# Kernel optimization log

Hardware: AMD Instinct MI355X
Metric: run time of the kernel (lower is better)

Reference implementation:

```python
import jax, jax.numpy as jnp
import numpy as np

TOP_K = 8
NEG_SLOPE = 0.2  # PyG GATConv default negative_slope


def setup_inputs() -> dict:
    key = jax.random.key(0)
    ks = jax.random.split(key, 8)
    B, C, T, D, H, KD = 16, 64, 128, 256, 8, 32
    s = 1.0 / np.sqrt(D)
    return {
        "x": jax.random.normal(ks[0], (B, C, T, D), jnp.float32),
        "static_adj": jax.random.normal(ks[1], (C, C), jnp.float32),
        "w_q": jax.random.normal(ks[2], (KD, D), jnp.float32) * s,
        "w_k": jax.random.normal(ks[3], (KD, D), jnp.float32) * s,
        "gat_lin": jax.random.normal(ks[4], (H * D, D), jnp.float32) * s,  # shared lin_src/lin_dst
        "att_src": jax.random.normal(ks[5], (H, D), jnp.float32) * s,
        "att_dst": jax.random.normal(ks[6], (H, D), jnp.float32) * s,
        "gat_bias": jnp.zeros((D,), jnp.float32),
    }


def reference(x, static_adj, w_q, w_k, gat_lin, att_src, att_dst, gat_bias):
    B, C, T, D = x.shape
    H = att_src.shape[0]
    kd = w_q.shape[0]

    # ---- dynamic adjacency ----
    h = x.mean(axis=2)                                   # [B,C,D] temporal summary
    q = h @ w_q.T                                        # [B,C,KD]
    k = h @ w_k.T                                        # [B,C,KD]
    sim = jnp.einsum('bik,bjk->bij', q, k) / np.float32(np.sqrt(kd))
    delta_a = jnp.tanh(sim)                              # [B,C,C]
    adaptive = static_adj[None] + delta_a                # [B,C,C]

    # top-k per row -> sparse mask (edge: row i = source, col j = target, per dense_to_sparse)
    _, idx = jax.lax.top_k(jnp.abs(adaptive), TOP_K)     # [B,C,K]
    mask = jnp.any(jax.nn.one_hot(idx, C, dtype=bool), axis=-2)  # [B,C,C]
    mask = mask | jnp.eye(C, dtype=bool)                 # GATConv add_self_loops=True

    # ---- GAT message passing (dense masked attention, graph shared across T) ----
    xt = jnp.swapaxes(x, 1, 2)                           # [B,T,C,D]
    wx = (xt @ gat_lin.T).reshape(B, T, C, H, D)         # [B,T,C,H,F]
    a_s = jnp.einsum('btchf,hf->btch', wx, att_src)      # source term
    a_d = jnp.einsum('btchf,hf->btch', wx, att_dst)      # target term
    # e[b,t,i,j,h]: edge source i -> target j
    e = a_s[:, :, :, None, :] + a_d[:, :, None, :, :]
    e = jax.nn.leaky_relu(e, NEG_SLOPE)
    e = jnp.where(mask[:, None, :, :, None], e, -jnp.inf)
    alpha = jax.nn.softmax(e, axis=2)                    # softmax over incoming sources i per target j
    out = jnp.einsum('btijh,btihf->btjhf', alpha, wx)    # aggregate messages
    out = out.mean(axis=3) + gat_bias                    # concat=False -> mean heads, add bias
    x_updated = jnp.swapaxes(out, 1, 2)                  # [B,C,T,D]
    return x_updated, delta_a
```

## Files before the change

### kernel.cpp

```cpp
#include <hip/hip_runtime.h>

typedef _Float16 h2_t __attribute__((ext_vector_type(2)));
typedef _Float16 h4_t __attribute__((ext_vector_type(4)));
typedef _Float16 h8_t __attribute__((ext_vector_type(8)));
typedef __fp16 fp16x2 __attribute__((ext_vector_type(2)));
typedef float f32x16 __attribute__((ext_vector_type(16)));


__device__ __forceinline__ h2_t pkrtz(float a, float b) {
  union { fp16x2 f; h2_t h; } u;
  u.f = __builtin_amdgcn_cvt_pkrtz(a, b);
  return u.h;
}

__device__ __forceinline__ unsigned pk_u(float a, float b) {
  union { fp16x2 f; unsigned u; } z;
  z.f = __builtin_amdgcn_cvt_pkrtz(a, b);
  return z.u;
}

__device__ __forceinline__ h8_t mk8(unsigned w0, unsigned w1, unsigned w2, unsigned w3) {
  union { unsigned u[4]; h8_t h; } z;
  z.u[0] = w0; z.u[1] = w1; z.u[2] = w2; z.u[3] = w3;
  return z.h;
}

__device__ __forceinline__ float fdot2_(h2_t a, h2_t b, float c) {
#if __has_builtin(__builtin_amdgcn_fdot2)
  return __builtin_amdgcn_fdot2(a, b, c, false);
#else
  return fmaf((float)a[0], (float)b[0], fmaf((float)a[1], (float)b[1], c));
#endif
}

__device__ __forceinline__ h2_t u2h(unsigned u) {
  union { unsigned u; h2_t h; } x; x.u = u; return x.h;
}

__global__ void k_hmean(const float* __restrict__ x, float* __restrict__ h) {
  int bc = blockIdx.x;
  int d = threadIdx.x;
  const float* xp = x + (size_t)bc * (128 * 256) + d;
  float s = 0.f;
  #pragma unroll 8
  for (int t = 0; t < 128; ++t) s += xp[(size_t)t * 256];
  h[bc * 256 + d] = s * (1.f / 128.f);
}

__global__ void k_qk(const float* __restrict__ h, const float* __restrict__ wq,
                     const float* __restrict__ wk, float* __restrict__ q,
                     float* __restrict__ k) {
  int gid = blockIdx.x * 256 + threadIdx.x;
  int isK = gid >> 15;
  int e = gid & 32767;
  int kk = e & 31;
  int bi = e >> 5;
  const float4* h4 = (const float4*)(h + bi * 256);
  const float4* w4 = (const float4*)((isK ? wk : wq) + kk * 256);
  float s = 0.f;
  #pragma unroll 4
  for (int d = 0; d < 64; ++d) {
    float4 a = h4[d], bv = w4[d];
    s = fmaf(a.x, bv.x, s); s = fmaf(a.y, bv.y, s);
    s = fmaf(a.z, bv.z, s); s = fmaf(a.w, bv.w, s);
  }
  (isK ? k : q)[e] = s;
}

__global__ void k_adj(const float* __restrict__ q, const float* __restrict__ k,
                      const float* __restrict__ sadj, float* __restrict__ dout,
                      unsigned long long* __restrict__ cmask) {
  __shared__ float qs[64][33], ks[64][33];
  __shared__ float ad[64][65];
  __shared__ unsigned long long rowm[64];
  int b = blockIdx.x, tid = threadIdx.x;
  for (int r = 0; r < 8; ++r) {
    int idx = r * 256 + tid;
    qs[idx >> 5][idx & 31] = q[b * 2048 + idx];
    ks[idx >> 5][idx & 31] = k[b * 2048 + idx];
  }
  __syncthreads();
  const float rs = 0.17677669529663687f;
  for (int r = 0; r < 16; ++r) {
    int idx = r * 256 + tid;
    int i = idx >> 6, j = idx & 63;
    float s = 0.f;
    #pragma unroll 8
    for (int kk = 0; kk < 32; ++kk) s = fmaf(qs[i][kk], ks[j][kk], s);
    float dv = tanhf(s * rs);
    dout[b * 4096 + idx] = dv;
    ad[i][j] = sadj[idx] + dv;
  }
  __syncthreads();
  if (tid < 64) {
    unsigned long long sel = 0ull;
    for (int p = 0; p < 8; ++p) {
      float best = -1.f; int bj = 0;
      for (int j = 0; j < 64; ++j) {
        if ((sel >> j) & 1ull) continue;
        float v = fabsf(ad[tid][j]);
        if (v > best) { best = v; bj = j; }
      }
      sel |= 1ull << bj;
    }
    rowm[tid] = sel;
  }
  __syncthreads();
  if (tid < 64) {
    unsigned long long cmv = 1ull << tid;
    for (int i = 0; i < 64; ++i) cmv |= ((rowm[i] >> tid) & 1ull) << i;
    cmask[b * 64 + tid] = cmv;
  }
}

__global__ void k_vsd(const float* __restrict__ glin, const float* __restrict__ asrc,
                      const float* __restrict__ adst, _Float16* __restrict__ vsd16) {
  int hh = blockIdx.x, d = threadIdx.x;
  const float* gb = glin + (size_t)hh * 65536;
  float s = 0.f, t = 0.f;
  for (int f = 0; f < 256; ++f) {
    float g = gb[f * 256 + d];
    s = fmaf(asrc[hh * 256 + f], g, s);
    t = fmaf(adst[hh * 256 + f], g, t);
  }
  vsd16[hh * 256 + d] = (_Float16)s;
  vsd16[(8 + hh) * 256 + d] = (_Float16)t;
}

__global__ void k_grearr(const float* __restrict__ g, _Float16* __restrict__ o) {
  int gid = blockIdx.x * 256 + threadIdx.x;
  int lane = gid & 63;
  int fg = (gid >> 6) & 3;
  int FID = gid >> 8;
  int ft = FID & 1, kk = (FID >> 1) & 3, s = FID >> 3;
  int h = s >> 2, dc = s & 3;
  int l5 = lane & 31, hi = lane >> 5;
  int f = fg * 64 + ft * 32 + l5;
  int d0 = dc * 64 + kk * 16 + hi * 8;
  const float* src = g + ((size_t)(h * 256 + f) << 8) + d0;
  float4 a = *(const float4*)src;
  float4 bq = *(const float4*)(src + 4);
  h8_t v;
  v[0] = (_Float16)a.x;  v[1] = (_Float16)a.y;  v[2] = (_Float16)a.z;  v[3] = (_Float16)a.w;
  v[4] = (_Float16)bq.x; v[5] = (_Float16)bq.y; v[6] = (_Float16)bq.z; v[7] = (_Float16)bq.w;
  *(h8_t*)(o + (size_t)gid * 8) = v;
}

__global__ __launch_bounds__(512) void k_main(
    const float* __restrict__ x, const _Float16* __restrict__ vsd16,
    const unsigned long long* __restrict__ cmask,
    const _Float16* __restrict__ g16r, const float* __restrict__ bias,
    float* __restrict__ out)
{
  __shared__ __align__(16) char LDS[69632];
  char* XR  = LDS;
  char* PT  = LDS;
  char* RED = LDS;
  float* ASp = (float*)(LDS + 65536);
  float* ADp = (float*)(LDS + 67584);

  const int tid = threadIdx.x;
  const int lane = tid & 63;
  const int w = __builtin_amdgcn_readfirstlane(tid >> 6);
  const int hi = lane >> 5;
  const int l5 = lane & 31;
  const int l7 = lane & 7;
  const int mg = w & 1;
  const int fg = w >> 1;
  const int bt = blockIdx.x;
  const int b = bt >> 7, t = bt & 127;

  const char* gb0 = (const char*)g16r + fg * 1024 + lane * 16;

  h8_t GA[8], GB[8];
  #pragma unroll
  for (int q = 0; q < 8; ++q) GA[q] = *(const h8_t*)(gb0 + q * 4096);

  #pragma unroll
  for (int r = 0; r < 8; ++r) {
    int i = w * 8 + r;
    const float4 v = *(const float4*)(x + (((size_t)(b * 64 + i) * 128 + t) << 8) + lane * 4);
    h2_t p0 = pkrtz(v.x, v.y);
    h2_t p1 = pkrtz(v.z, v.w);
    h4_t hv; hv[0] = p0[0]; hv[1] = p0[1]; hv[2] = p1[0]; hv[3] = p1[1];
    int db = lane >> 1;
    int off = i * 512 + (((db & 24) | ((db ^ (i & 7)) & 7)) << 4) + ((lane & 1) << 3);
    *(h4_t*)(XR + off) = hv;
  }
  __syncthreads();

  h8_t Af[16];
  {
    int i = mg * 32 + l5;
    #pragma unroll
    for (int k = 0; k < 16; ++k) {
      int db = k * 2 + hi;
      Af[k] = *(const h8_t*)(XR + i * 512 + (((db & 24) | ((db ^ l7) & 7)) << 4));
    }
  }

  {
    float a_s = 0.f, a_d = 0.f;
    const unsigned* vsp = (const unsigned*)vsd16 + w * 128;
    const unsigned* vdp = (const unsigned*)vsd16 + (8 + w) * 128;
    #pragma unroll 4
    for (int db = 0; db < 32; ++db) {
      h8_t xv = *(const h8_t*)(XR + lane * 512 + (((db & 24) | ((db ^ l7) & 7)) << 4));
      #pragma unroll
      for (int c = 0; c < 4; ++c) {
        h2_t x2; x2[0] = xv[c * 2]; x2[1] = xv[c * 2 + 1];
        a_s = fdot2_(x2, u2h(vsp[db * 4 + c]), a_s);
        a_d = fdot2_(x2, u2h(vdp[db * 4 + c]), a_d);
      }
    }
    ASp[w * 64 + lane] = a_s;
    ADp[w * 64 + lane] = a_d;
  }
  __syncthreads();

  {
    const unsigned long long cmj = cmask[b * 64 + lane];
    const float adj = ADp[w * 64 + lane];
    const float* asr = ASp + w * 64;
    float ssum = 0.f;
    #pragma unroll 8
    for (int i = 0; i < 64; ++i) {
      float e = asr[i] + adj;
      e = fmaxf(e, 0.f) + 0.2f * fminf(e, 0.f);
      e = ((cmj >> i) & 1ull) ? e : -1e30f;
      ssum += exp2f(e * 1.44269504f);
    }
    const float rinv = 1.f / ssum;
    #pragma unroll
    for (int c = 0; c < 8; ++c) {
      float vv[8];
      #pragma unroll
      for (int e8 = 0; e8 < 8; ++e8) {
        int i = c * 8 + e8;
        float e = asr[i] + adj;
        e = fmaxf(e, 0.f) + 0.2f * fminf(e, 0.f);
        e = ((cmj >> i) & 1ull) ? e : -1e30f;
        vv[e8] = exp2f(e * 1.44269504f) * rinv;
      }
      *(h8_t*)(PT + w * 8192 + lane * 128 + ((c ^ l7) << 4)) =
          mk8(pk_u(vv[0], vv[1]), pk_u(vv[2], vv[3]),
              pk_u(vv[4], vv[5]), pk_u(vv[6], vv[7]));
    }
  }
  __syncthreads();

  f32x16 acc00 = {}, acc01 = {}, acc10 = {}, acc11 = {};

  #pragma unroll 1
  for (int h = 0; h < 8; ++h) {
    f32x16 d0 = {}, d1 = {};

    #pragma unroll
    for (int dc = 0; dc < 4; ++dc) {
      const int s = h * 4 + dc;
      const int sp = (s < 31) ? s + 1 : 31;
      const char* gpp = gb0 + (size_t)sp * 32768;
      if ((dc & 1) == 0) {
        #pragma unroll
        for (int q = 0; q < 8; ++q) GB[q] = *(const h8_t*)(gpp + q * 4096);
        #pragma unroll
        for (int kk = 0; kk < 4; ++kk) {
          d0 = __builtin_amdgcn_mfma_f32_32x32x16_f16(Af[dc * 4 + kk], GA[kk * 2 + 0], d0, 0, 0, 0);
          d1 = __builtin_amdgcn_mfma_f32_32x32x16_f16(Af[dc * 4 + kk], GA[kk * 2 + 1], d1, 0, 0, 0);
        }
      } else {
        #pragma unroll
        for (int q = 0; q < 8; ++q) GA[q] = *(const h8_t*)(gpp + q * 4096);
        #pragma unroll
        for (int kk = 0; kk < 4; ++kk) {
          d0 = __builtin_amdgcn_mfma_f32_32x32x16_f16(Af[dc * 4 + kk], GB[kk * 2 + 0], d0, 0, 0, 0);
          d1 = __builtin_amdgcn_mfma_f32_32x32x16_f16(Af[dc * 4 + kk], GB[kk * 2 + 1], d1, 0, 0, 0);
        }
      }
    }

    h8_t B2[2][2];
    {
      const bool H = (hi != 0);
      #pragma unroll
      for (int ft = 0; ft < 2; ++ft) {
        const f32x16& dd = ft ? d1 : d0;
        unsigned P0 = pk_u(dd[0], dd[1]),  P1 = pk_u(dd[2], dd[3]);
        unsigned P2 = pk_u(dd[4], dd[5]),  P3 = pk_u(dd[6], dd[7]);
        unsigned P4 = pk_u(dd[8], dd[9]),  P5 = pk_u(dd[10], dd[11]);
        unsigned P6 = pk_u(dd[12], dd[13]), P7 = pk_u(dd[14], dd[15]);
        {
          unsigned Pa = H ? P2 : P0, Pb = H ? P3 : P1;
          unsigned Qa = H ? P0 : P2, Qb = H ? P1 : P3;
          unsigned S0 = (unsigned)__shfl_xor((int)Qa, 32);
          unsigned S1 = (unsigned)__shfl_xor((int)Qb, 32);
          B2[0][ft] = mk8(H ? S0 : Pa, H ? S1 : Pb, H ? Pa : S0, H ? Pb : S1);
        }
        {
          unsigned Pa = H ? P6 : P4, Pb = H ? P7 : P5;
          unsigned Qa = H ? P4 : P6, Qb = H ? P5 : P7;
          unsigned S0 = (unsigned)__shfl_xor((int)Qa, 32);
          unsigned S1 = (unsigned)__shfl_xor((int)Qb, 32);
          B2[1][ft] = mk8(H ? S0 : Pa, H ? S1 : Pb, H ? Pa : S0, H ? Pb : S1);
        }
      }
    }

    h8_t A2[2][2];
    #pragma unroll
    for (int jt = 0; jt < 2; ++jt)
      #pragma unroll
      for (int kbl = 0; kbl < 2; ++kbl) {
        int c = mg * 4 + kbl * 2 + hi;
        A2[jt][kbl] = *(const h8_t*)(PT + h * 8192 + (jt * 32 + l5) * 128 + ((c ^ (l5 & 7)) << 4));
      }

    acc00 = __builtin_amdgcn_mfma_f32_32x32x16_f16(A2[0][0], B2[0][0], acc00, 0, 0, 0);
    acc00 = __builtin_amdgcn_mfma_f32_32x32x16_f16(A2[0][1], B2[1][0], acc00, 0, 0, 0);
    acc01 = __builtin_amdgcn_mfma_f32_32x32x16_f16(A2[0][0], B2[0][1], acc01, 0, 0, 0);
    acc01 = __builtin_amdgcn_mfma_f32_32x32x16_f16(A2[0][1], B2[1][1], acc01, 0, 0, 0);
    acc10 = __builtin_amdgcn_mfma_f32_32x32x16_f16(A2[1][0], B2[0][0], acc10, 0, 0, 0);
    acc10 = __builtin_amdgcn_mfma_f32_32x32x16_f16(A2[1][1], B2[1][0], acc10, 0, 0, 0);
    acc11 = __builtin_amdgcn_mfma_f32_32x32x16_f16(A2[1][0], B2[0][1], acc11, 0, 0, 0);
    acc11 = __builtin_amdgcn_mfma_f32_32x32x16_f16(A2[1][1], B2[1][1], acc11, 0, 0, 0);
  }

  __syncthreads();
  if (mg == 1) {
    #pragma unroll
    for (int jt = 0; jt < 2; ++jt)
      #pragma unroll
      for (int ft = 0; ft < 2; ++ft) {
        const f32x16& a = jt ? (ft ? acc11 : acc10) : (ft ? acc01 : acc00);
        #pragma unroll
        for (int rq = 0; rq < 4; ++rq) {
          float4 v; v.x = a[rq*4+0]; v.y = a[rq*4+1]; v.z = a[rq*4+2]; v.w = a[rq*4+3];
          *(float4*)(RED + (((((fg*2+jt)*2+ft)*4 + rq)*64 + lane) << 4)) = v;
        }
      }
  }
  __syncthreads();
  if (mg == 0) {
    const float bi0 = bias[fg * 64 + l5];
    const float bi1 = bias[fg * 64 + 32 + l5];
    float* ob = out + ((size_t)(b * 64) * 128 + t) * 256;
    #pragma unroll
    for (int jt = 0; jt < 2; ++jt)
      #pragma unroll
      for (int ft = 0; ft < 2; ++ft) {
        const f32x16& a = jt ? (ft ? acc11 : acc10) : (ft ? acc01 : acc00);
        const float bv = ft ? bi1 : bi0;
        const int fcol = fg * 64 + ft * 32 + l5;
        #pragma unroll
        for (int rq = 0; rq < 4; ++rq) {
          float4 p = *(const float4*)(RED + (((((fg*2+jt)*2+ft)*4 + rq)*64 + lane) << 4));
          #pragma unroll
          for (int rr = 0; rr < 4; ++rr) {
            int j = jt * 32 + rr + 8 * rq + 4 * hi;
            float sum = a[rq*4+rr] + ((const float*)&p)[rr];
            ob[(size_t)j * 32768 + fcol] = sum * 0.125f + bv;
          }
        }
      }
  }
}

extern "C" void kernel_launch(void* const* d_in, const int* in_sizes, int n_in,
                              void* d_out, int out_size, void* d_ws, size_t ws_size,
                              hipStream_t stream) {
  const float* x    = (const float*)d_in[0];
  const float* sadj = (const float*)d_in[1];
  const float* wq   = (const float*)d_in[2];
  const float* wk   = (const float*)d_in[3];
  const float* glin = (const float*)d_in[4];
  const float* asrc = (const float*)d_in[5];
  const float* adst = (const float*)d_in[6];
  const float* bias = (const float*)d_in[7];

  float* out = (float*)d_out;
  float* delta_out = out + (size_t)16 * 64 * 128 * 256;

  char* ws = (char*)d_ws;
  float* h   = (float*)(ws + 0);
  float* q   = (float*)(ws + 1048576);
  float* k   = (float*)(ws + 1179648);
  unsigned long long* cm = (unsigned long long*)(ws + 1310720);
  _Float16* vsd16 = (_Float16*)(ws + 1318912);
  _Float16* g16r  = (_Float16*)(ws + 1327104);

  hipLaunchKernelGGL(k_hmean,  dim3(1024), dim3(256), 0, stream, x, h);
  hipLaunchKernelGGL(k_qk,     dim3(256),  dim3(256), 0, stream, h, wq, wk, q, k);
  hipLaunchKernelGGL(k_adj,    dim3(16),   dim3(256), 0, stream, q, k, sadj, delta_out, cm);
  hipLaunchKernelGGL(k_vsd,    dim3(8),    dim3(256), 0, stream, glin, asrc, adst, vsd16);
  hipLaunchKernelGGL(k_grearr, dim3(256),  dim3(256), 0, stream, glin, g16r);
  hipLaunchKernelGGL(k_main,   dim3(2048), dim3(512), 0, stream, x, vsd16, cm, g16r, bias, out);
}
```

Measured before the change: 361.3 us.

## Process two timesteps per block, each wave pair owning one timestep

```diff
diff --git a/kernel.cpp b/kernel.cpp
--- a/kernel.cpp
+++ b/kernel.cpp
@@ -152,12 +152,11 @@
     const _Float16* __restrict__ g16r, const float* __restrict__ bias,
     float* __restrict__ out)
 {
-  __shared__ __align__(16) char LDS[69632];
-  char* XR  = LDS;
-  char* PT  = LDS;
-  char* RED = LDS;
-  float* ASp = (float*)(LDS + 65536);
-  float* ADp = (float*)(LDS + 67584);
+  __shared__ __align__(16) char LDS[139264];
+  char* XT  = LDS;
+  char* PT  = LDS + 65536;
+  float* ASp = (float*)(LDS + 131072);
+  float* ADp = (float*)(LDS + 135168);
 
   const int tid = threadIdx.x;
   const int lane = tid & 63;
@@ -165,10 +164,12 @@
   const int hi = lane >> 5;
   const int l5 = lane & 31;
   const int l7 = lane & 7;
-  const int mg = w & 1;
+  const int tg = w & 1;
   const int fg = w >> 1;
   const int bt = blockIdx.x;
-  const int b = bt >> 7, t = bt & 127;
+  const int b = bt >> 6;
+  const int t0 = (bt & 63) * 2;
+  const int t = t0 + tg;
 
   const char* gb0 = (const char*)g16r + fg * 1024 + lane * 16;
 
@@ -176,174 +177,186 @@
   #pragma unroll
   for (int q = 0; q < 8; ++q) GA[q] = *(const h8_t*)(gb0 + q * 4096);
 
-  #pragma unroll
-  for (int r = 0; r < 8; ++r) {
-    int i = w * 8 + r;
-    const float4 v = *(const float4*)(x + (((size_t)(b * 64 + i) * 128 + t) << 8) + lane * 4);
-    h2_t p0 = pkrtz(v.x, v.y);
-    h2_t p1 = pkrtz(v.z, v.w);
-    h4_t hv; hv[0] = p0[0]; hv[1] = p0[1]; hv[2] = p1[0]; hv[3] = p1[1];
-    int db = lane >> 1;
-    int off = i * 512 + (((db & 24) | ((db ^ (i & 7)) & 7)) << 4) + ((lane & 1) << 3);
-    *(h4_t*)(XR + off) = hv;
+  const unsigned long long cmj = cmask[b * 64 + lane];
+
+  {
+    char* XL = XT + tg * 32768;
+    const int rb = fg * 16;
+    #pragma unroll
+    for (int r = 0; r < 16; ++r) {
+      int i = rb + r;
+      const float4 v = *(const float4*)(x + (((size_t)(b * 64 + i) * 128 + t) << 8) + lane * 4);
+      h2_t p0 = pkrtz(v.x, v.y);
+      h2_t p1 = pkrtz(v.z, v.w);
+      h4_t hv; hv[0] = p0[0]; hv[1] = p0[1]; hv[2] = p1[0]; hv[3] = p1[1];
+      int db = lane >> 1;
+      int off = i * 512 + (((db & 24) | ((db ^ (i & 7)) & 7)) << 4) + ((lane & 1) << 3);
+      *(h4_t*)(XL + off) = hv;
+    }
   }
   __syncthreads();
 
-  h8_t Af[16];
   {
-    int i = mg * 32 + l5;
-    #pragma unroll
-    for (int k = 0; k < 16; ++k) {
-      int db = k * 2 + hi;
-      Af[k] = *(const h8_t*)(XR + i * 512 + (((db & 24) | ((db ^ l7) & 7)) << 4));
-    }
-  }
-
-  {
-    float a_s = 0.f, a_d = 0.f;
-    const unsigned* vsp = (const unsigned*)vsd16 + w * 128;
-    const unsigned* vdp = (const unsigned*)vsd16 + (8 + w) * 128;
+    const char* XL = XT + tg * 32768;
+    const int hp = w >> 1;
+    float s0 = 0.f, d0v = 0.f, s1 = 0.f, d1v = 0.f;
+    const unsigned* vsp0 = (const unsigned*)vsd16 + hp * 128;
+    const unsigned* vdp0 = (const unsigned*)vsd16 + (8 + hp) * 128;
+    const unsigned* vsp1 = (const unsigned*)vsd16 + (hp + 4) * 128;
+    const unsigned* vdp1 = (const unsigned*)vsd16 + (12 + hp) * 128;
     #pragma unroll 4
     for (int db = 0; db < 32; ++db) {
-      h8_t xv = *(const h8_t*)(XR + lane * 512 + (((db & 24) | ((db ^ l7) & 7)) << 4));
+      h8_t xv = *(const h8_t*)(XL + lane * 512 + (((db & 24) | ((db ^ l7) & 7)) << 4));
       #pragma unroll
       for (int c = 0; c < 4; ++c) {
         h2_t x2; x2[0] = xv[c * 2]; x2[1] = xv[c * 2 + 1];
-        a_s = fdot2_(x2, u2h(vsp[db * 4 + c]), a_s);
-        a_d = fdot2_(x2, u2h(vdp[db * 4 + c]), a_d);
+        s0  = fdot2_(x2, u2h(vsp0[db * 4 + c]), s0);
+        d0v = fdot2_(x2, u2h(vdp0[db * 4 + c]), d0v);
+        s1  = fdot2_(x2, u2h(vsp1[db * 4 + c]), s1);
+        d1v = fdot2_(x2, u2h(vdp1[db * 4 + c]), d1v);
       }
     }
-    ASp[w * 64 + lane] = a_s;
-    ADp[w * 64 + lane] = a_d;
+    ASp[tg * 512 + hp * 64 + lane] = s0;
+    ADp[tg * 512 + hp * 64 + lane] = d0v;
+    ASp[tg * 512 + (hp + 4) * 64 + lane] = s1;
+    ADp[tg * 512 + (hp + 4) * 64 + lane] = d1v;
   }
   __syncthreads();
 
-  {
-    const unsigned long long cmj = cmask[b * 64 + lane];
-    const float adj = ADp[w * 64 + lane];
-    const float* asr = ASp + w * 64;
-    float ssum = 0.f;
-    #pragma unroll 8
-    for (int i = 0; i < 64; ++i) {
-      float e = asr[i] + adj;
-      e = fmaxf(e, 0.f) + 0.2f * fminf(e, 0.f);
-      e = ((cmj >> i) & 1ull) ? e : -1e30f;
-      ssum += exp2f(e * 1.44269504f);
-    }
-    const float rinv = 1.f / ssum;
-    #pragma unroll
-    for (int c = 0; c < 8; ++c) {
-      float vv[8];
-      #pragma unroll
-      for (int e8 = 0; e8 < 8; ++e8) {
-        int i = c * 8 + e8;
+  f32x16 acc00 = {}, acc01 = {}, acc10 = {}, acc11 = {};
+
+  #pragma unroll 1
+  for (int rnd = 0; rnd < 2; ++rnd) {
+    {
+      const int hp = w >> 1;
+      const int h = rnd * 4 + hp;
+      const float adj = ADp[tg * 512 + h * 64 + lane];
+      const float* asr = ASp + tg * 512 + h * 64;
+      float ssum = 0.f;
+      #pragma unroll 8
+      for (int i = 0; i < 64; ++i) {
         float e = asr[i] + adj;
         e = fmaxf(e, 0.f) + 0.2f * fminf(e, 0.f);
         e = ((cmj >> i) & 1ull) ? e : -1e30f;
-        vv[e8] = exp2f(e * 1.44269504f) * rinv;
-      }
-      *(h8_t*)(PT + w * 8192 + lane * 128 + ((c ^ l7) << 4)) =
-          mk8(pk_u(vv[0], vv[1]), pk_u(vv[2], vv[3]),
-              pk_u(vv[4], vv[5]), pk_u(vv[6], vv[7]));
+        ssum += exp2f(e * 1.44269504f);
+      }
+      const float rinv = 1.f / ssum;
+      char* pslot = PT + (hp * 2 + tg) * 8192;
+      #pragma unroll
+      for (int c = 0; c < 8; ++c) {
+        float vv[8];
+        #pragma unroll
+        for (int e8 = 0; e8 < 8; ++e8) {
+          int i = c * 8 + e8;
+          float e = asr[i] + adj;
+          e = fmaxf(e, 0.f) + 0.2f * fminf(e, 0.f);
+          e = ((cmj >> i) & 1ull) ? e : -1e30f;
+          vv[e8] = exp2f(e * 1.44269504f) * rinv;
+        }
+        *(h8_t*)(pslot + lane * 128 + ((c ^ l7) << 4)) =
+            mk8(pk_u(vv[0], vv[1]), pk_u(vv[2], vv[3]),
+                pk_u(vv[4], vv[5]), pk_u(vv[6], vv[7]));
+      }
     }
-  }
-  __syncthreads();
-
-  f32x16 acc00 = {}, acc01 = {}, acc10 = {}, acc11 = {};
-
-  #pragma unroll 1
-  for (int h = 0; h < 8; ++h) {
-    f32x16 d0 = {}, d1 = {};
-
-    #pragma unroll
-    for (int dc = 0; dc < 4; ++dc) {
-      const int s = h * 4 + dc;
-      const int sp = (s < 31) ? s + 1 : 31;
-      const char* gpp = gb0 + (size_t)sp * 32768;
-      if ((dc & 1) == 0) {
-        #pragma unroll
-        for (int q = 0; q < 8; ++q) GB[q] = *(const h8_t*)(gpp + q * 4096);
+    __syncthreads();
+
+    #pragma unroll 1
+    for (int hh = 0; hh < 4; ++hh) {
+      const int h = rnd * 4 + hh;
+      f32x16 d00 = {}, d01 = {}, d10 = {}, d11 = {};
+      const char* XL = XT + tg * 32768;
+
+      #pragma unroll
+      for (int dc = 0; dc < 4; ++dc) {
+        const int s = h * 4 + dc;
+        const int sp = (s < 31) ? s + 1 : 31;
+        const char* gpp = gb0 + (size_t)sp * 32768;
+        h8_t a0[4], a1[4];
         #pragma unroll
         for (int kk = 0; kk < 4; ++kk) {
-          d0 = __builtin_amdgcn_mfma_f32_32x32x16_f16(Af[dc * 4 + kk], GA[kk * 2 + 0], d0, 0, 0, 0);
-          d1 = __builtin_amdgcn_mfma_f32_32x32x16_f16(Af[dc * 4 + kk], GA[kk * 2 + 1], d1, 0, 0, 0);
+          int db = dc * 8 + kk * 2 + hi;
+          int sw = (((db & 24) | ((db ^ l7) & 7)) << 4);
+          a0[kk] = *(const h8_t*)(XL + l5 * 512 + sw);
+          a1[kk] = *(const h8_t*)(XL + (32 + l5) * 512 + sw);
         }
-      } else {
+        if ((dc & 1) == 0) {
+          #pragma unroll
+          for (int q = 0; q < 8; ++q) GB[q] = *(const h8_t*)(gpp + q * 4096);
+          #pragma unroll
+          for (int kk = 0; kk < 4; ++kk) {
+            d00 = __builtin_amdgcn_mfma_f32_32x32x16_f16(a0[kk], GA[kk * 2 + 0], d00, 0, 0, 0);
+            d01 = __builtin_amdgcn_mfma_f32_32x32x16_f16(a0[kk], GA[kk * 2 + 1], d01, 0, 0, 0);
+            d10 = __builtin_amdgcn_mfma_f32_32x32x16_f16(a1[kk], GA[kk * 2 + 0], d10, 0, 0, 0);
+            d11 = __builtin_amdgcn_mfma_f32_32x32x16_f16(a1[kk], GA[kk * 2 + 1], d11, 0, 0, 0);
+          }
+        } else {
+          #pragma unroll
+          for (int q = 0; q < 8; ++q) GA[q] = *(const h8_t*)(gpp + q * 4096);
+          #pragma unroll
+          for (int kk = 0; kk < 4; ++kk) {
+            d00 = __builtin_amdgcn_mfma_f32_32x32x16_f16(a0[kk], GB[kk * 2 + 0], d00, 0, 0, 0);
+            d01 = __builtin_amdgcn_mfma_f32_32x32x16_f16(a0[kk], GB[kk * 2 + 1], d01, 0, 0, 0);
+            d10 = __builtin_amdgcn_mfma_f32_32x32x16_f16(a1[kk], GB[kk * 2 + 0], d10, 0, 0, 0);
+            d11 = __builtin_amdgcn_mfma_f32_32x32x16_f16(a1[kk], GB[kk * 2 + 1], d11, 0, 0, 0);
+          }
+        }
+      }
+
+      h8_t B2[4][2];
+      {
+        const bool H = (hi != 0);
         #pragma unroll
-        for (int q = 0; q < 8; ++q) GA[q] = *(const h8_t*)(gpp + q * 4096);
+        for (int m = 0; m < 2; ++m) {
+          #pragma unroll
+          for (int ft = 0; ft < 2; ++ft) {
+            const f32x16& dd = m ? (ft ? d11 : d10) : (ft ? d01 : d00);
+            unsigned P0 = pk_u(dd[0], dd[1]),  P1 = pk_u(dd[2], dd[3]);
+            unsigned P2 = pk_u(dd[4], dd[5]),  P3 = pk_u(dd[6], dd[7]);
+            unsigned P4 = pk_u(dd[8], dd[9]),  P5 = pk_u(dd[10], dd[11]);
+            unsigned P6 = pk_u(dd[12], dd[13]), P7 = pk_u(dd[14], dd[15]);
+            {
+              unsigned Pa = H ? P2 : P0, Pb = H ? P3 : P1;
+              unsigned Qa = H ? P0 : P2, Qb = H ? P1 : P3;
+              unsigned S0 = (unsigned)__shfl_xor((int)Qa, 32);
+              unsigned S1 = (unsigned)__shfl_xor((int)Qb, 32);
+              B2[m * 2 + 0][ft] = mk8(H ? S0 : Pa, H ? S1 : Pb, H ? Pa : S0, H ? Pb : S1);
+            }
+            {
+              unsigned Pa = H ? P6 : P4, Pb = H ? P7 : P5;
+              unsigned Qa = H ? P4 : P6, Qb = H ? P5 : P7;
+              unsigned S0 = (unsigned)__shfl_xor((int)Qa, 32);
+              unsigned S1 = (unsigned)__shfl_xor((int)Qb, 32);
+              B2[m * 2 + 1][ft] = mk8(H ? S0 : Pa, H ? S1 : Pb, H ? Pa : S0, H ? Pb : S1);
+            }
+          }
+        }
+      }
+
+      const char* pslot = PT + (hh * 2 + tg) * 8192;
+      h8_t A2[2][4];
+      #pragma unroll
+      for (int jt = 0; jt < 2; ++jt)
         #pragma unroll
-        for (int kk = 0; kk < 4; ++kk) {
-          d0 = __builtin_amdgcn_mfma_f32_32x32x16_f16(Af[dc * 4 + kk], GB[kk * 2 + 0], d0, 0, 0, 0);
-          d1 = __builtin_amdgcn_mfma_f32_32x32x16_f16(Af[dc * 4 + kk], GB[kk * 2 + 1], d1, 0, 0, 0);
+        for (int kbl = 0; kbl < 4; ++kbl) {
+          int c = kbl * 2 + hi;
+          A2[jt][kbl] = *(const h8_t*)(pslot + (jt * 32 + l5) * 128 + ((c ^ (l5 & 7)) << 4));
         }
+
+      #pragma unroll
+      for (int kbl = 0; kbl < 4; ++kbl) {
+        acc00 = __builtin_amdgcn_mfma_f32_32x32x16_f16(A2[0][kbl], B2[kbl][0], acc00, 0, 0, 0);
+        acc01 = __builtin_amdgcn_mfma_f32_32x32x16_f16(A2[0][kbl], B2[kbl][1], acc01, 0, 0, 0);
+        acc10 = __builtin_amdgcn_mfma_f32_32x32x16_f16(A2[1][kbl], B2[kbl][0], acc10, 0, 0, 0);
+        acc11 = __builtin_amdgcn_mfma_f32_32x32x16_f16(A2[1][kbl], B2[kbl][1], acc11, 0, 0, 0);
       }
     }
-
-    h8_t B2[2][2];
-    {
-      const bool H = (hi != 0);
-      #pragma unroll
-      for (int ft = 0; ft < 2; ++ft) {
-        const f32x16& dd = ft ? d1 : d0;
-        unsigned P0 = pk_u(dd[0], dd[1]),  P1 = pk_u(dd[2], dd[3]);
-        unsigned P2 = pk_u(dd[4], dd[5]),  P3 = pk_u(dd[6], dd[7]);
-        unsigned P4 = pk_u(dd[8], dd[9]),  P5 = pk_u(dd[10], dd[11]);
-        unsigned P6 = pk_u(dd[12], dd[13]), P7 = pk_u(dd[14], dd[15]);
-        {
-          unsigned Pa = H ? P2 : P0, Pb = H ? P3 : P1;
-          unsigned Qa = H ? P0 : P2, Qb = H ? P1 : P3;
-          unsigned S0 = (unsigned)__shfl_xor((int)Qa, 32);
-          unsigned S1 = (unsigned)__shfl_xor((int)Qb, 32);
-          B2[0][ft] = mk8(H ? S0 : Pa, H ? S1 : Pb, H ? Pa : S0, H ? Pb : S1);
-        }
-        {
-          unsigned Pa = H ? P6 : P4, Pb = H ? P7 : P5;
-          unsigned Qa = H ? P4 : P6, Qb = H ? P5 : P7;
-          unsigned S0 = (unsigned)__shfl_xor((int)Qa, 32);
-          unsigned S1 = (unsigned)__shfl_xor((int)Qb, 32);
-          B2[1][ft] = mk8(H ? S0 : Pa, H ? S1 : Pb, H ? Pa : S0, H ? Pb : S1);
-        }
-      }
-    }
-
-    h8_t A2[2][2];
-    #pragma unroll
-    for (int jt = 0; jt < 2; ++jt)
-      #pragma unroll
-      for (int kbl = 0; kbl < 2; ++kbl) {
-        int c = mg * 4 + kbl * 2 + hi;
-        A2[jt][kbl] = *(const h8_t*)(PT + h * 8192 + (jt * 32 + l5) * 128 + ((c ^ (l5 & 7)) << 4));
-      }
-
-    acc00 = __builtin_amdgcn_mfma_f32_32x32x16_f16(A2[0][0], B2[0][0], acc00, 0, 0, 0);
-    acc00 = __builtin_amdgcn_mfma_f32_32x32x16_f16(A2[0][1], B2[1][0], acc00, 0, 0, 0);
-    acc01 = __builtin_amdgcn_mfma_f32_32x32x16_f16(A2[0][0], B2[0][1], acc01, 0, 0, 0);
-    acc01 = __builtin_amdgcn_mfma_f32_32x32x16_f16(A2[0][1], B2[1][1], acc01, 0, 0, 0);
-    acc10 = __builtin_amdgcn_mfma_f32_32x32x16_f16(A2[1][0], B2[0][0], acc10, 0, 0, 0);
-    acc10 = __builtin_amdgcn_mfma_f32_32x32x16_f16(A2[1][1], B2[1][0], acc10, 0, 0, 0);
-    acc11 = __builtin_amdgcn_mfma_f32_32x32x16_f16(A2[1][0], B2[0][1], acc11, 0, 0, 0);
-    acc11 = __builtin_amdgcn_mfma_f32_32x32x16_f16(A2[1][1], B2[1][1], acc11, 0, 0, 0);
-  }
-
-  __syncthreads();
-  if (mg == 1) {
-    #pragma unroll
-    for (int jt = 0; jt < 2; ++jt)
-      #pragma unroll
-      for (int ft = 0; ft < 2; ++ft) {
-        const f32x16& a = jt ? (ft ? acc11 : acc10) : (ft ? acc01 : acc00);
-        #pragma unroll
-        for (int rq = 0; rq < 4; ++rq) {
-          float4 v; v.x = a[rq*4+0]; v.y = a[rq*4+1]; v.z = a[rq*4+2]; v.w = a[rq*4+3];
-          *(float4*)(RED + (((((fg*2+jt)*2+ft)*4 + rq)*64 + lane) << 4)) = v;
-        }
-      }
-  }
-  __syncthreads();
-  if (mg == 0) {
+    __syncthreads();
+  }
+
+  {
     const float bi0 = bias[fg * 64 + l5];
     const float bi1 = bias[fg * 64 + 32 + l5];
-    float* ob = out + ((size_t)(b * 64) * 128 + t) * 256;
+    float* ob = out + (((size_t)(b * 64) * 128 + t) << 8);
     #pragma unroll
     for (int jt = 0; jt < 2; ++jt)
       #pragma unroll
@@ -352,15 +365,12 @@
         const float bv = ft ? bi1 : bi0;
         const int fcol = fg * 64 + ft * 32 + l5;
         #pragma unroll
-        for (int rq = 0; rq < 4; ++rq) {
-          float4 p = *(const float4*)(RED + (((((fg*2+jt)*2+ft)*4 + rq)*64 + lane) << 4));
+        for (int rq = 0; rq < 4; ++rq)
           #pragma unroll
           for (int rr = 0; rr < 4; ++rr) {
-            int j = jt * 32 + rr + 8 * rq + 4 * hi;
-            float sum = a[rq*4+rr] + ((const float*)&p)[rr];
-            ob[(size_t)j * 32768 + fcol] = sum * 0.125f + bv;
+            int j = jt * 32 + rq * 8 + hi * 4 + rr;
+            ob[(size_t)j * 32768 + fcol] = a[rq * 4 + rr] * 0.125f + bv;
           }
-        }
       }
   }
 }
@@ -393,5 +403,5 @@
   hipLaunchKernelGGL(k_adj,    dim3(16),   dim3(256), 0, stream, q, k, sadj, delta_out, cm);
   hipLaunchKernelGGL(k_vsd,    dim3(8),    dim3(256), 0, stream, glin, asrc, adst, vsd16);
   hipLaunchKernelGGL(k_grearr, dim3(256),  dim3(256), 0, stream, glin, g16r);
-  hipLaunchKernelGGL(k_main,   dim3(2048), dim3(512), 0, stream, x, vsd16, cm, g16r, bias, out);
-}
+  hipLaunchKernelGGL(k_main,   dim3(1024), dim3(512), 0, stream, x, vsd16, cm, g16r, bias, out);
+}
```

Result: slower. 456.7 us (+26.4%).
